# Kernel tuning notes

Measured on AMD Instinct MI355X. Metric: run time of the kernel, lower is better.

## Reference

```python
import jax, jax.numpy as jnp
import numpy as np

TEXTURE_W, SHAPE_W, INTENSITY_W = 1.0, 0.5, 1.0
EPS = 1e-08


def _conv2d_same(x, k):
    # x: [B,1,H,W], k: [1,1,3,3], zero padding 1 (SAME)
    return jax.lax.conv_general_dilated(
        x, k, window_strides=(1, 1), padding='SAME',
        dimension_numbers=('NCHW', 'OIHW', 'NCHW'))


def _box_mean(x):
    # mean over 3x3 zero-padded window == F.unfold(k=3,pad=1).mean(dim=1) for C=1
    k = jnp.ones((1, 1, 3, 3), x.dtype) / 9.0
    return _conv2d_same(x, k)


def _local_variance(x):
    # mean((patch - patch_mean)^2) == E[x^2] - E[x]^2 over the padded 3x3 window
    m = _box_mean(x)
    m2 = _box_mean(x * x)
    return m2 - m * m


def _intensity_loss(inp, out, mask):
    ms = mask.sum() + EPS
    im = (inp * mask).sum() / ms
    om = (out * mask).sum() / ms
    di, do = inp - im, out - om
    iv = (di * di * mask).sum() / ms
    ov = (do * do * mask).sum() / ms
    isk = (di ** 3 * mask).sum() / (ms * (iv ** 1.5 + EPS))
    osk = (do ** 3 * mask).sum() / (ms * (ov ** 1.5 + EPS))
    iku = (di ** 4 * mask).sum() / (ms * (iv ** 2 + EPS))
    oku = (do ** 4 * mask).sum() / (ms * (ov ** 2 + EPS))
    return (im - om) ** 2 + (iv - ov) ** 2 + (isk - osk) ** 2 + (iku - oku) ** 2


def _texture_loss(inp, out, mask):
    it = _local_variance(inp)
    ot = _local_variance(out)
    return jnp.abs(ot * mask - it * mask).mean()


def _shape_loss(inp, out, mask):
    lap = jnp.array([[0., 1., 0.], [1., -4., 1.], [0., 1., 0.]], inp.dtype).reshape(1, 1, 3, 3)
    il = _conv2d_same(inp, lap)
    ol = _conv2d_same(out, lap)
    return jnp.abs(ol * mask - il * mask).mean()


def setup_inputs() -> dict:
    key = jax.random.key(0)
    k1, k2, k3 = jax.random.split(key, 3)
    shape = (32, 1, 512, 512)
    return {
        'input_img': jax.random.normal(k1, shape, jnp.float32),
        'output_img': jax.random.normal(k2, shape, jnp.float32),
        'roi_mask': jax.random.uniform(k3, shape, jnp.float32),
    }


def reference(input_img, output_img, roi_mask):
    intensity = _intensity_loss(input_img, output_img, roi_mask)
    texture = _texture_loss(input_img, output_img, roi_mask)
    shape = _shape_loss(input_img, output_img, roi_mask)
    total = INTENSITY_W * intensity + TEXTURE_W * texture + SHAPE_W * shape
    # stacked [intensity, texture, shape, total] (dict values in original order)
    return jnp.stack([intensity, texture, shape, total])
```

## Files before the change

kernel.cpp:

```cpp
#include <hip/hip_runtime.h>
#include <math.h>

#define H 512
#define W 512
#define BAND 8
#define STAGE (BAND + 2)
#define NQ 11

typedef __attribute__((address_space(3))) void       lds_void;
typedef const __attribute__((address_space(1))) void g_void;

__device__ __forceinline__ void async_copy16(const float* g, float* l) {
    __builtin_amdgcn_global_load_lds((g_void*)g, (lds_void*)l, 16, 0, 0);
}

__device__ __forceinline__ void load10(const float* row, int x0, float* a) {
    float4 u = *(const float4*)&row[x0];
    float4 v = *(const float4*)&row[x0 + 4];
    a[0] = (x0 == 0) ? 0.0f : row[x0 - 1];
    a[1] = u.x; a[2] = u.y; a[3] = u.z; a[4] = u.w;
    a[5] = v.x; a[6] = v.y; a[7] = v.z; a[8] = v.w;
    a[9] = (x0 + 8 == W) ? 0.0f : row[x0 + 8];
}

__global__ __launch_bounds__(256) void radiomics_main(
    const float* __restrict__ inp, const float* __restrict__ outp,
    const float* __restrict__ mask, double* __restrict__ partials)
{
    __shared__ float lds[2][STAGE][W];

    const int tid  = threadIdx.x;
    const int lane = tid & 63;
    const int wib  = tid >> 6;
    const int blk  = blockIdx.x;
    const int b    = blk >> 6;
    const int band = blk & 63;
    const int y0   = band * BAND;
    const size_t off = (size_t)b * H * W;
    const int x0   = lane * 8;

    for (int s = wib; s < 2 * STAGE * 2; s += 4) {
        const int img = s / (2 * STAGE);
        const int rem = s - img * (2 * STAGE);
        const int rs  = rem >> 1;
        const int g   = rem & 1;
        const int y   = y0 - 1 + rs;
        float* dst = &lds[img][rs][g * 256];
        if (y < 0 || y >= H) {
            *(float4*)&dst[lane * 4] = make_float4(0.f, 0.f, 0.f, 0.f);
        } else {
            const float* src = (img ? outp : inp) + off + (size_t)y * W + g * 256 + lane * 4;
            async_copy16(src, dst);
        }
    }

    const int r0 = y0 + 2 * wib;
    float Mk[16];
    {
        const float4* p = (const float4*)(mask + off + (size_t)r0 * W + x0);
        float4 a = p[0], c = p[1];
        const float4* q = (const float4*)(mask + off + (size_t)(r0 + 1) * W + x0);
        float4 d = q[0], e = q[1];
        Mk[0]=a.x; Mk[1]=a.y; Mk[2]=a.z; Mk[3]=a.w; Mk[4]=c.x; Mk[5]=c.y; Mk[6]=c.z; Mk[7]=c.w;
        Mk[8]=d.x; Mk[9]=d.y; Mk[10]=d.z; Mk[11]=d.w; Mk[12]=e.x; Mk[13]=e.y; Mk[14]=e.z; Mk[15]=e.w;
    }

    __syncthreads();

    const float inv9 = 1.0f / 9.0f;
    float acc[NQ];
    #pragma unroll
    for (int q = 0; q < NQ; q++) acc[q] = 0.0f;

    #pragma unroll
    for (int cr = 0; cr < 2; cr++) {
        const int rs = 2 * wib + cr + 1;
        const float* mrow = &Mk[cr * 8];
        float tvI[8], lpI[8];

        {
            float A[10], B[10], C[10];
            load10(lds[0][rs - 1], x0, A);
            load10(lds[0][rs],     x0, B);
            load10(lds[0][rs + 1], x0, C);
            float c1[10], c2[10];
            #pragma unroll
            for (int j = 0; j < 10; j++) {
                c1[j] = A[j] + B[j] + C[j];
                c2[j] = fmaf(A[j], A[j], fmaf(B[j], B[j], C[j] * C[j]));
            }
            #pragma unroll
            for (int j = 0; j < 8; j++) {
                float s1 = c1[j] + c1[j+1] + c1[j+2];
                float s2 = c2[j] + c2[j+1] + c2[j+2];
                float mn = s1 * inv9;
                tvI[j] = fmaf(-mn, mn, s2 * inv9);
                lpI[j] = A[j+1] + C[j+1] + B[j] + B[j+2] - 4.0f * B[j+1];
                float m = mrow[j];
                acc[0] += m;
                float x = B[j+1];
                float t = x * m; acc[1] += t; t *= x; acc[2] += t; t *= x; acc[3] += t; t *= x; acc[4] += t;
            }
        }
        {
            float A[10], B[10], C[10];
            load10(lds[1][rs - 1], x0, A);
            load10(lds[1][rs],     x0, B);
            load10(lds[1][rs + 1], x0, C);
            float c1[10], c2[10];
            #pragma unroll
            for (int j = 0; j < 10; j++) {
                c1[j] = A[j] + B[j] + C[j];
                c2[j] = fmaf(A[j], A[j], fmaf(B[j], B[j], C[j] * C[j]));
            }
            #pragma unroll
            for (int j = 0; j < 8; j++) {
                float s1 = c1[j] + c1[j+1] + c1[j+2];
                float s2 = c2[j] + c2[j+1] + c2[j+2];
                float mn = s1 * inv9;
                float tv = fmaf(-mn, mn, s2 * inv9);
                float lp = A[j+1] + C[j+1] + B[j] + B[j+2] - 4.0f * B[j+1];
                float m = mrow[j];
                acc[9]  += fabsf(tv * m - tvI[j] * m);
                acc[10] += fabsf(lp * m - lpI[j] * m);
                float x = B[j+1];
                float t = x * m; acc[5] += t; t *= x; acc[6] += t; t *= x; acc[7] += t; t *= x; acc[8] += t;
            }
        }
    }

    #pragma unroll
    for (int q = 0; q < NQ; q++) {
        float v = acc[q];
        #pragma unroll
        for (int o = 32; o > 0; o >>= 1) v += __shfl_down(v, o);
        acc[q] = v;
    }
    __syncthreads();
    float* rf = (float*)lds;
    if (lane == 0) {
        #pragma unroll
        for (int q = 0; q < NQ; q++) rf[wib * NQ + q] = acc[q];
    }
    __syncthreads();
    if (tid < NQ) {
        double s = (double)rf[tid] + (double)rf[NQ + tid]
                 + (double)rf[2 * NQ + tid] + (double)rf[3 * NQ + tid];
        partials[(size_t)blk * NQ + tid] = s;
    }
}

__global__ __launch_bounds__(256) void radiomics_final(
    const double* __restrict__ partials, int nblk, float* __restrict__ out4, double inv_n)
{
    const int tid = threadIdx.x;
    const int lane = tid & 63;
    const int w = tid >> 6;
    double q[NQ];
    #pragma unroll
    for (int k = 0; k < NQ; k++) q[k] = 0.0;
    for (int i = tid; i < nblk; i += 256) {
        #pragma unroll
        for (int k = 0; k < NQ; k++) q[k] += partials[(size_t)i * NQ + k];
    }
    #pragma unroll
    for (int k = 0; k < NQ; k++) {
        #pragma unroll
        for (int o = 32; o > 0; o >>= 1) q[k] += __shfl_down(q[k], o);
    }
    __shared__ double red[4][NQ];
    if (lane == 0) {
        #pragma unroll
        for (int k = 0; k < NQ; k++) red[w][k] = q[k];
    }
    __syncthreads();
    if (tid == 0) {
        double s[NQ];
        #pragma unroll
        for (int k = 0; k < NQ; k++) s[k] = red[0][k] + red[1][k] + red[2][k] + red[3][k];
        const double EPS = 1e-8;
        double S0 = s[0];
        double ms = S0 + EPS;
        double im = s[1] / ms, om = s[5] / ms;
        double im2 = im * im, im3 = im2 * im, im4 = im2 * im2;
        double om2 = om * om, om3 = om2 * om, om4 = om2 * om2;
        double di2 = s[2] - 2.0*im*s[1] + im2*S0;
        double do2 = s[6] - 2.0*om*s[5] + om2*S0;
        double iv = di2 / ms, ov = do2 / ms;
        double di3 = s[3] - 3.0*im*s[2] + 3.0*im2*s[1] - im3*S0;
        double do3 = s[7] - 3.0*om*s[6] + 3.0*om2*s[5] - om3*S0;
        double isk = di3 / (ms * (iv * sqrt(iv) + EPS));
        double osk = do3 / (ms * (ov * sqrt(ov) + EPS));
        double di4 = s[4] - 4.0*im*s[3] + 6.0*im2*s[2] - 4.0*im3*s[1] + im4*S0;
        double do4 = s[8] - 4.0*om*s[7] + 6.0*om2*s[6] - 4.0*om3*s[5] + om4*S0;
        double iku = di4 / (ms * (iv * iv + EPS));
        double oku = do4 / (ms * (ov * ov + EPS));
        double intensity = (im-om)*(im-om) + (iv-ov)*(iv-ov)
                         + (isk-osk)*(isk-osk) + (iku-oku)*(iku-oku);
        double texture = s[9]  * inv_n;
        double shape   = s[10] * inv_n;
        double total = intensity + texture + 0.5 * shape;
        out4[0] = (float)intensity;
        out4[1] = (float)texture;
        out4[2] = (float)shape;
        out4[3] = (float)total;
    }
}

extern "C" void kernel_launch(void* const* d_in, const int* in_sizes, int n_in,
                              void* d_out, int out_size, void* d_ws, size_t ws_size,
                              hipStream_t stream) {
    const float* inp  = (const float*)d_in[0];
    const float* outp = (const float*)d_in[1];
    const float* mask = (const float*)d_in[2];
    const int total = in_sizes[0];
    const int nimg  = total / (H * W);
    const int nblk  = nimg * (H / BAND);
    double* partials = (double*)d_ws;

    radiomics_main<<<nblk, 256, 0, stream>>>(inp, outp, mask, partials);
    const double inv_n = 1.0 / (double)total;
    radiomics_final<<<1, 256, 0, stream>>>(partials, nblk, (float*)d_out, inv_n);
}
```

Measured before the change: 131.1 us.

## Make blocks persistent over four bands with double-buffered async LDS staging

Reduces band height from 8 to 4 rows and launches a fixed 1024 blocks that each process four bands. The next band's rows are fetched asynchronously into a second LDS buffer while the current one is computed, so global loads overlap with arithmetic. The halo overhead per band rises (6 staged rows for 4 output rows instead of 10 for 8), and the grid size and 32-image count are now hardcoded.

```diff
diff --git a/kernel.cpp b/kernel.cpp
--- a/kernel.cpp
+++ b/kernel.cpp
@@ -3,9 +3,11 @@
 
 #define H 512
 #define W 512
-#define BAND 8
-#define STAGE (BAND + 2)
+#define BAND 4
+#define STAGE 6
 #define NQ 11
+#define NBLK 1024
+#define ROUNDS 4
 
 typedef __attribute__((address_space(3))) void       lds_void;
 typedef const __attribute__((address_space(1))) void g_void;
@@ -27,62 +29,67 @@
     const float* __restrict__ inp, const float* __restrict__ outp,
     const float* __restrict__ mask, double* __restrict__ partials)
 {
-    __shared__ float lds[2][STAGE][W];
+    __shared__ float lds[2][2][STAGE][W];
 
     const int tid  = threadIdx.x;
     const int lane = tid & 63;
     const int wib  = tid >> 6;
-    const int blk  = blockIdx.x;
-    const int b    = blk >> 6;
-    const int band = blk & 63;
-    const int y0   = band * BAND;
-    const size_t off = (size_t)b * H * W;
     const int x0   = lane * 8;
 
-    for (int s = wib; s < 2 * STAGE * 2; s += 4) {
-        const int img = s / (2 * STAGE);
-        const int rem = s - img * (2 * STAGE);
-        const int rs  = rem >> 1;
-        const int g   = rem & 1;
-        const int y   = y0 - 1 + rs;
-        float* dst = &lds[img][rs][g * 256];
-        if (y < 0 || y >= H) {
-            *(float4*)&dst[lane * 4] = make_float4(0.f, 0.f, 0.f, 0.f);
-        } else {
-            const float* src = (img ? outp : inp) + off + (size_t)y * W + g * 256 + lane * 4;
-            async_copy16(src, dst);
-        }
-    }
-
-    const int r0 = y0 + 2 * wib;
-    float Mk[16];
-    {
-        const float4* p = (const float4*)(mask + off + (size_t)r0 * W + x0);
+    float acc[NQ];
+    #pragma unroll
+    for (int q = 0; q < NQ; q++) acc[q] = 0.0f;
+    float Mk[8], Mn[8];
+    const float inv9 = 1.0f / 9.0f;
+
+    auto stage_band = [&](int band_id, int buf) {
+        const int bimg = band_id >> 7;
+        const int y0   = (band_id & 127) * BAND;
+        const size_t off = (size_t)bimg * H * W;
+        #pragma unroll
+        for (int s = wib; s < 2 * STAGE * 2; s += 4) {
+            const int img = (s >= 2 * STAGE);
+            const int rem = s - img * 2 * STAGE;
+            const int rs  = rem >> 1;
+            const int g   = rem & 1;
+            const int y   = y0 - 1 + rs;
+            float* dst = &lds[buf][img][rs][g * 256];
+            if (y < 0 || y >= H) {
+                *(float4*)&dst[lane * 4] = make_float4(0.f, 0.f, 0.f, 0.f);
+            } else {
+                const float* src = (img ? outp : inp) + off + (size_t)y * W + g * 256 + lane * 4;
+                async_copy16(src, dst);
+            }
+        }
+    };
+    auto load_mask8 = [&](int band_id, float* M) {
+        const int bimg = band_id >> 7;
+        const int y    = (band_id & 127) * BAND + wib;
+        const float4* p = (const float4*)(mask + (size_t)bimg * H * W + (size_t)y * W + x0);
         float4 a = p[0], c = p[1];
-        const float4* q = (const float4*)(mask + off + (size_t)(r0 + 1) * W + x0);
-        float4 d = q[0], e = q[1];
-        Mk[0]=a.x; Mk[1]=a.y; Mk[2]=a.z; Mk[3]=a.w; Mk[4]=c.x; Mk[5]=c.y; Mk[6]=c.z; Mk[7]=c.w;
-        Mk[8]=d.x; Mk[9]=d.y; Mk[10]=d.z; Mk[11]=d.w; Mk[12]=e.x; Mk[13]=e.y; Mk[14]=e.z; Mk[15]=e.w;
-    }
-
-    __syncthreads();
-
-    const float inv9 = 1.0f / 9.0f;
-    float acc[NQ];
-    #pragma unroll
-    for (int q = 0; q < NQ; q++) acc[q] = 0.0f;
-
-    #pragma unroll
-    for (int cr = 0; cr < 2; cr++) {
-        const int rs = 2 * wib + cr + 1;
-        const float* mrow = &Mk[cr * 8];
+        M[0]=a.x; M[1]=a.y; M[2]=a.z; M[3]=a.w; M[4]=c.x; M[5]=c.y; M[6]=c.z; M[7]=c.w;
+    };
+
+    stage_band(blockIdx.x, 0);
+    load_mask8(blockIdx.x, Mk);
+
+    int cur = 0;
+    #pragma unroll
+    for (int k = 0; k < ROUNDS; k++) {
+        __syncthreads();
+
+        if (k < ROUNDS - 1) {
+            stage_band(blockIdx.x + (k + 1) * NBLK, cur ^ 1);
+            load_mask8(blockIdx.x + (k + 1) * NBLK, Mn);
+        }
+
+        const int rs = wib + 1;
         float tvI[8], lpI[8];
-
         {
             float A[10], B[10], C[10];
-            load10(lds[0][rs - 1], x0, A);
-            load10(lds[0][rs],     x0, B);
-            load10(lds[0][rs + 1], x0, C);
+            load10(lds[cur][0][rs - 1], x0, A);
+            load10(lds[cur][0][rs],     x0, B);
+            load10(lds[cur][0][rs + 1], x0, C);
             float c1[10], c2[10];
             #pragma unroll
             for (int j = 0; j < 10; j++) {
@@ -96,7 +103,7 @@
                 float mn = s1 * inv9;
                 tvI[j] = fmaf(-mn, mn, s2 * inv9);
                 lpI[j] = A[j+1] + C[j+1] + B[j] + B[j+2] - 4.0f * B[j+1];
-                float m = mrow[j];
+                float m = Mk[j];
                 acc[0] += m;
                 float x = B[j+1];
                 float t = x * m; acc[1] += t; t *= x; acc[2] += t; t *= x; acc[3] += t; t *= x; acc[4] += t;
@@ -104,9 +111,9 @@
         }
         {
             float A[10], B[10], C[10];
-            load10(lds[1][rs - 1], x0, A);
-            load10(lds[1][rs],     x0, B);
-            load10(lds[1][rs + 1], x0, C);
+            load10(lds[cur][1][rs - 1], x0, A);
+            load10(lds[cur][1][rs],     x0, B);
+            load10(lds[cur][1][rs + 1], x0, C);
             float c1[10], c2[10];
             #pragma unroll
             for (int j = 0; j < 10; j++) {
@@ -120,13 +127,19 @@
                 float mn = s1 * inv9;
                 float tv = fmaf(-mn, mn, s2 * inv9);
                 float lp = A[j+1] + C[j+1] + B[j] + B[j+2] - 4.0f * B[j+1];
-                float m = mrow[j];
+                float m = Mk[j];
                 acc[9]  += fabsf(tv * m - tvI[j] * m);
                 acc[10] += fabsf(lp * m - lpI[j] * m);
                 float x = B[j+1];
                 float t = x * m; acc[5] += t; t *= x; acc[6] += t; t *= x; acc[7] += t; t *= x; acc[8] += t;
             }
         }
+
+        if (k < ROUNDS - 1) {
+            #pragma unroll
+            for (int j = 0; j < 8; j++) Mk[j] = Mn[j];
+        }
+        cur ^= 1;
     }
 
     #pragma unroll
@@ -146,7 +159,7 @@
     if (tid < NQ) {
         double s = (double)rf[tid] + (double)rf[NQ + tid]
                  + (double)rf[2 * NQ + tid] + (double)rf[3 * NQ + tid];
-        partials[(size_t)blk * NQ + tid] = s;
+        partials[(size_t)blockIdx.x * NQ + tid] = s;
     }
 }
 
@@ -214,11 +227,9 @@
     const float* outp = (const float*)d_in[1];
     const float* mask = (const float*)d_in[2];
     const int total = in_sizes[0];
-    const int nimg  = total / (H * W);
-    const int nblk  = nimg * (H / BAND);
     double* partials = (double*)d_ws;
 
-    radiomics_main<<<nblk, 256, 0, stream>>>(inp, outp, mask, partials);
+    radiomics_main<<<NBLK, 256, 0, stream>>>(inp, outp, mask, partials);
     const double inv_n = 1.0 / (double)total;
-    radiomics_final<<<1, 256, 0, stream>>>(partials, nblk, (float*)d_out, inv_n);
-}
+    radiomics_final<<<1, 256, 0, stream>>>(partials, NBLK, (float*)d_out, inv_n);
+}
```

Measured after the change: 133.2 us. Within noise of the previous version (+1.6%).

## Replace LDS-staged row bands with direct global loads per two-row block

Applied to the files above, without the earlier changes.

Drops the LDS staging of 10-row bands and instead has each thread load its own 3-row, 6-wide neighbourhood straight from global memory, relying on L2/L1 to serve the halo re-reads. Each block now covers only 2 rows with 4 pixels per thread, giving 8192 blocks in a slab-interleaved order, and the final reduction kernel widens to 1024 threads. The aim is to remove the LDS round-trip and barrier and to raise parallelism, at the cost of about 3x redundant row reads through cache and a partials array that is four times larger. The block count is hard-coded to 8192, which assumes 32 images of 512x512.

```diff
diff --git a/kernel.cpp b/kernel.cpp
--- a/kernel.cpp
+++ b/kernel.cpp
@@ -3,130 +3,87 @@
 
 #define H 512
 #define W 512
-#define BAND 8
-#define STAGE (BAND + 2)
 #define NQ 11
-
-typedef __attribute__((address_space(3))) void       lds_void;
-typedef const __attribute__((address_space(1))) void g_void;
-
-__device__ __forceinline__ void async_copy16(const float* g, float* l) {
-    __builtin_amdgcn_global_load_lds((g_void*)g, (lds_void*)l, 16, 0, 0);
-}
-
-__device__ __forceinline__ void load10(const float* row, int x0, float* a) {
-    float4 u = *(const float4*)&row[x0];
-    float4 v = *(const float4*)&row[x0 + 4];
-    a[0] = (x0 == 0) ? 0.0f : row[x0 - 1];
-    a[1] = u.x; a[2] = u.y; a[3] = u.z; a[4] = u.w;
-    a[5] = v.x; a[6] = v.y; a[7] = v.z; a[8] = v.w;
-    a[9] = (x0 + 8 == W) ? 0.0f : row[x0 + 8];
-}
+#define NBLK 8192
 
 __global__ __launch_bounds__(256) void radiomics_main(
     const float* __restrict__ inp, const float* __restrict__ outp,
     const float* __restrict__ mask, double* __restrict__ partials)
 {
-    __shared__ float lds[2][STAGE][W];
-
     const int tid  = threadIdx.x;
     const int lane = tid & 63;
     const int wib  = tid >> 6;
     const int blk  = blockIdx.x;
-    const int b    = blk >> 6;
-    const int band = blk & 63;
-    const int y0   = band * BAND;
-    const size_t off = (size_t)b * H * W;
-    const int x0   = lane * 8;
+    const int slab = blk & 7;
+    const int idx  = blk >> 3;
+    const int img  = idx >> 5;
+    const int rp   = idx & 31;
+    const int r    = slab * 64 + rp * 2 + (tid >> 7);
+    const int x0   = (tid & 127) * 4;
 
-    for (int s = wib; s < 2 * STAGE * 2; s += 4) {
-        const int img = s / (2 * STAGE);
-        const int rem = s - img * (2 * STAGE);
-        const int rs  = rem >> 1;
-        const int g   = rem & 1;
-        const int y   = y0 - 1 + rs;
-        float* dst = &lds[img][rs][g * 256];
-        if (y < 0 || y >= H) {
-            *(float4*)&dst[lane * 4] = make_float4(0.f, 0.f, 0.f, 0.f);
-        } else {
-            const float* src = (img ? outp : inp) + off + (size_t)y * W + g * 256 + lane * 4;
-            async_copy16(src, dst);
-        }
+    const size_t off = (size_t)img * H * W;
+    const float* Ab = inp  + off;
+    const float* Bb = outp + off;
+
+    float a[3][6], b[3][6];
+    #pragma unroll
+    for (int dy = 0; dy < 3; dy++) {
+        const int y = r - 1 + dy;
+        const bool yok = (y >= 0) && (y < H);
+        const float* pa = Ab + (size_t)(yok ? y : 0) * W + x0;
+        const float* pb = Bb + (size_t)(yok ? y : 0) * W + x0;
+        float4 va = yok ? *(const float4*)pa : make_float4(0.f,0.f,0.f,0.f);
+        float4 vb = yok ? *(const float4*)pb : make_float4(0.f,0.f,0.f,0.f);
+        float la = (yok && x0 > 0)     ? pa[-1] : 0.0f;
+        float lb = (yok && x0 > 0)     ? pb[-1] : 0.0f;
+        float ra = (yok && x0 + 4 < W) ? pa[4]  : 0.0f;
+        float rb = (yok && x0 + 4 < W) ? pb[4]  : 0.0f;
+        a[dy][0]=la; a[dy][1]=va.x; a[dy][2]=va.y; a[dy][3]=va.z; a[dy][4]=va.w; a[dy][5]=ra;
+        b[dy][0]=lb; b[dy][1]=vb.x; b[dy][2]=vb.y; b[dy][3]=vb.z; b[dy][4]=vb.w; b[dy][5]=rb;
     }
-
-    const int r0 = y0 + 2 * wib;
-    float Mk[16];
-    {
-        const float4* p = (const float4*)(mask + off + (size_t)r0 * W + x0);
-        float4 a = p[0], c = p[1];
-        const float4* q = (const float4*)(mask + off + (size_t)(r0 + 1) * W + x0);
-        float4 d = q[0], e = q[1];
-        Mk[0]=a.x; Mk[1]=a.y; Mk[2]=a.z; Mk[3]=a.w; Mk[4]=c.x; Mk[5]=c.y; Mk[6]=c.z; Mk[7]=c.w;
-        Mk[8]=d.x; Mk[9]=d.y; Mk[10]=d.z; Mk[11]=d.w; Mk[12]=e.x; Mk[13]=e.y; Mk[14]=e.z; Mk[15]=e.w;
-    }
-
-    __syncthreads();
+    float4 m4 = *(const float4*)(mask + off + (size_t)r * W + x0);
+    const float mk[4] = { m4.x, m4.y, m4.z, m4.w };
 
     const float inv9 = 1.0f / 9.0f;
     float acc[NQ];
     #pragma unroll
     for (int q = 0; q < NQ; q++) acc[q] = 0.0f;
 
+    float c1[6], c2[6], tvI[4], lpI[4];
     #pragma unroll
-    for (int cr = 0; cr < 2; cr++) {
-        const int rs = 2 * wib + cr + 1;
-        const float* mrow = &Mk[cr * 8];
-        float tvI[8], lpI[8];
-
-        {
-            float A[10], B[10], C[10];
-            load10(lds[0][rs - 1], x0, A);
-            load10(lds[0][rs],     x0, B);
-            load10(lds[0][rs + 1], x0, C);
-            float c1[10], c2[10];
-            #pragma unroll
-            for (int j = 0; j < 10; j++) {
-                c1[j] = A[j] + B[j] + C[j];
-                c2[j] = fmaf(A[j], A[j], fmaf(B[j], B[j], C[j] * C[j]));
-            }
-            #pragma unroll
-            for (int j = 0; j < 8; j++) {
-                float s1 = c1[j] + c1[j+1] + c1[j+2];
-                float s2 = c2[j] + c2[j+1] + c2[j+2];
-                float mn = s1 * inv9;
-                tvI[j] = fmaf(-mn, mn, s2 * inv9);
-                lpI[j] = A[j+1] + C[j+1] + B[j] + B[j+2] - 4.0f * B[j+1];
-                float m = mrow[j];
-                acc[0] += m;
-                float x = B[j+1];
-                float t = x * m; acc[1] += t; t *= x; acc[2] += t; t *= x; acc[3] += t; t *= x; acc[4] += t;
-            }
-        }
-        {
-            float A[10], B[10], C[10];
-            load10(lds[1][rs - 1], x0, A);
-            load10(lds[1][rs],     x0, B);
-            load10(lds[1][rs + 1], x0, C);
-            float c1[10], c2[10];
-            #pragma unroll
-            for (int j = 0; j < 10; j++) {
-                c1[j] = A[j] + B[j] + C[j];
-                c2[j] = fmaf(A[j], A[j], fmaf(B[j], B[j], C[j] * C[j]));
-            }
-            #pragma unroll
-            for (int j = 0; j < 8; j++) {
-                float s1 = c1[j] + c1[j+1] + c1[j+2];
-                float s2 = c2[j] + c2[j+1] + c2[j+2];
-                float mn = s1 * inv9;
-                float tv = fmaf(-mn, mn, s2 * inv9);
-                float lp = A[j+1] + C[j+1] + B[j] + B[j+2] - 4.0f * B[j+1];
-                float m = mrow[j];
-                acc[9]  += fabsf(tv * m - tvI[j] * m);
-                acc[10] += fabsf(lp * m - lpI[j] * m);
-                float x = B[j+1];
-                float t = x * m; acc[5] += t; t *= x; acc[6] += t; t *= x; acc[7] += t; t *= x; acc[8] += t;
-            }
-        }
+    for (int k = 0; k < 6; k++) {
+        c1[k] = a[0][k] + a[1][k] + a[2][k];
+        c2[k] = fmaf(a[0][k], a[0][k], fmaf(a[1][k], a[1][k], a[2][k] * a[2][k]));
+    }
+    #pragma unroll
+    for (int j = 0; j < 4; j++) {
+        float s1 = c1[j] + c1[j+1] + c1[j+2];
+        float s2 = c2[j] + c2[j+1] + c2[j+2];
+        float mn = s1 * inv9;
+        tvI[j] = fmaf(-mn, mn, s2 * inv9);
+        lpI[j] = a[0][j+1] + a[2][j+1] + a[1][j] + a[1][j+2] - 4.0f * a[1][j+1];
+        float m = mk[j];
+        acc[0] += m;
+        float x = a[1][j+1];
+        float t = x * m; acc[1] += t; t *= x; acc[2] += t; t *= x; acc[3] += t; t *= x; acc[4] += t;
+    }
+    #pragma unroll
+    for (int k = 0; k < 6; k++) {
+        c1[k] = b[0][k] + b[1][k] + b[2][k];
+        c2[k] = fmaf(b[0][k], b[0][k], fmaf(b[1][k], b[1][k], b[2][k] * b[2][k]));
+    }
+    #pragma unroll
+    for (int j = 0; j < 4; j++) {
+        float s1 = c1[j] + c1[j+1] + c1[j+2];
+        float s2 = c2[j] + c2[j+1] + c2[j+2];
+        float mn = s1 * inv9;
+        float tv = fmaf(-mn, mn, s2 * inv9);
+        float lp = b[0][j+1] + b[2][j+1] + b[1][j] + b[1][j+2] - 4.0f * b[1][j+1];
+        float m = mk[j];
+        acc[9]  += fabsf(tv * m - tvI[j] * m);
+        acc[10] += fabsf(lp * m - lpI[j] * m);
+        float x = b[1][j+1];
+        float t = x * m; acc[5] += t; t *= x; acc[6] += t; t *= x; acc[7] += t; t *= x; acc[8] += t;
     }
 
     #pragma unroll
@@ -136,21 +93,20 @@
         for (int o = 32; o > 0; o >>= 1) v += __shfl_down(v, o);
         acc[q] = v;
     }
-    __syncthreads();
-    float* rf = (float*)lds;
+    __shared__ float red[4][NQ];
     if (lane == 0) {
         #pragma unroll
-        for (int q = 0; q < NQ; q++) rf[wib * NQ + q] = acc[q];
+        for (int q = 0; q < NQ; q++) red[wib][q] = acc[q];
     }
     __syncthreads();
     if (tid < NQ) {
-        double s = (double)rf[tid] + (double)rf[NQ + tid]
-                 + (double)rf[2 * NQ + tid] + (double)rf[3 * NQ + tid];
+        double s = (double)red[0][tid] + (double)red[1][tid]
+                 + (double)red[2][tid] + (double)red[3][tid];
         partials[(size_t)blk * NQ + tid] = s;
     }
 }
 
-__global__ __launch_bounds__(256) void radiomics_final(
+__global__ __launch_bounds__(1024) void radiomics_final(
     const double* __restrict__ partials, int nblk, float* __restrict__ out4, double inv_n)
 {
     const int tid = threadIdx.x;
@@ -159,7 +115,7 @@
     double q[NQ];
     #pragma unroll
     for (int k = 0; k < NQ; k++) q[k] = 0.0;
-    for (int i = tid; i < nblk; i += 256) {
+    for (int i = tid; i < nblk; i += 1024) {
         #pragma unroll
         for (int k = 0; k < NQ; k++) q[k] += partials[(size_t)i * NQ + k];
     }
@@ -168,7 +124,7 @@
         #pragma unroll
         for (int o = 32; o > 0; o >>= 1) q[k] += __shfl_down(q[k], o);
     }
-    __shared__ double red[4][NQ];
+    __shared__ double red[16][NQ];
     if (lane == 0) {
         #pragma unroll
         for (int k = 0; k < NQ; k++) red[w][k] = q[k];
@@ -177,7 +133,12 @@
     if (tid == 0) {
         double s[NQ];
         #pragma unroll
-        for (int k = 0; k < NQ; k++) s[k] = red[0][k] + red[1][k] + red[2][k] + red[3][k];
+        for (int k = 0; k < NQ; k++) {
+            double t = 0.0;
+            #pragma unroll
+            for (int ww = 0; ww < 16; ww++) t += red[ww][k];
+            s[k] = t;
+        }
         const double EPS = 1e-8;
         double S0 = s[0];
         double ms = S0 + EPS;
@@ -214,11 +175,9 @@
     const float* outp = (const float*)d_in[1];
     const float* mask = (const float*)d_in[2];
     const int total = in_sizes[0];
-    const int nimg  = total / (H * W);
-    const int nblk  = nimg * (H / BAND);
     double* partials = (double*)d_ws;
 
-    radiomics_main<<<nblk, 256, 0, stream>>>(inp, outp, mask, partials);
+    radiomics_main<<<NBLK, 256, 0, stream>>>(inp, outp, mask, partials);
     const double inv_n = 1.0 / (double)total;
-    radiomics_final<<<1, 256, 0, stream>>>(partials, nblk, (float*)d_out, inv_n);
+    radiomics_final<<<1, 1024, 0, stream>>>(partials, NBLK, (float*)d_out, inv_n);
 }
```

After: 150.8 us. 1.15x slower.
